# Optimization experiments

Hardware: AMD Instinct MI355X
Metric: run time of the kernel (lower is better)

The kernel has to match this reference:

```python
import jax, jax.numpy as jnp
import numpy as np

N_OPCODES = 31
B, S, D = 64, 16, 1024
MAX_STEPS = 16


def setup_inputs() -> dict:
    key = jax.random.key(0)
    k1, k2, k3, k4 = jax.random.split(key, 4)
    return {
        "opcode_logits": jax.random.normal(k1, (B, S, N_OPCODES), dtype=jnp.float32),
        "operands": jax.random.normal(k2, (B, S, 4), dtype=jnp.float32),
        "signal": jax.random.normal(k3, (B, D), dtype=jnp.float32),
        "op_kernels": jax.random.normal(k4, (N_OPCODES, D, D), dtype=jnp.float32) * 0.01,
    }


def reference(opcode_logits, operands, signal, op_kernels):
    # opcode_logits: (B,S,O), operands: (B,S,4), signal: (B,D), op_kernels: (O,D,D)
    n_steps = min(opcode_logits.shape[1], MAX_STEPS)
    weights = jax.nn.softmax(opcode_logits, axis=-1)  # (B,S,O)

    # time-major inputs for scan: (n_steps, B, O) and (n_steps, B, 1)
    ws = jnp.swapaxes(weights[:, :n_steps], 0, 1)
    gate_logits = jnp.swapaxes(operands[:, :n_steps, 3:4], 0, 1)

    def step(h, inputs):
        w, gl = inputs  # (B,O), (B,1)
        gate = jax.nn.sigmoid(gl)
        # equivalent to h @ (sum_o w_o K_o) but never forms the (B,D,D) kernel
        transformed = jnp.einsum('bo,bd,odk->bk', w, h, op_kernels)
        h_new = gate * transformed + (1.0 - gate) * h
        return h_new, None

    h, _ = jax.lax.scan(step, signal, (ws, gate_logits))
    return h
```

## Files before the change

### kernel.cpp

```cpp
#include <hip/hip_runtime.h>
#include <cstddef>
#include <cstdint>

#define NB 64
#define ND 1024
#define NO 31
#define NSTEPS 16
#define KS 62
#define KT32 992
#define KC32 16

typedef _Float16 half8 __attribute__((ext_vector_type(8)));
typedef float floatx4 __attribute__((ext_vector_type(4)));

__global__ void softmax_k(const float* __restrict__ logits, float* __restrict__ W) {
    int row = blockIdx.x * blockDim.x + threadIdx.x;
    if (row >= NB * NSTEPS) return;
    const float* x = logits + (size_t)row * NO;
    float m = -1e30f;
    for (int o = 0; o < NO; ++o) m = fmaxf(m, x[o]);
    float e[NO]; float s = 0.f;
    for (int o = 0; o < NO; ++o) { e[o] = expf(x[o] - m); s += e[o]; }
    float inv = 1.0f / s;
    float* wo = W + (size_t)row * NO;
    for (int o = 0; o < NO; ++o) wo[o] = e[o] * inv;
}

__global__ __launch_bounds__(256) void kconv_k(const float* __restrict__ K,
                                               _Float16* __restrict__ Ktf) {
    __shared__ float tile[32 * 256];
    int kt  = blockIdx.x >> 2;
    int nb4 = blockIdx.x & 3;
    int tid = threadIdx.x;
    int lane = tid & 63, w = tid >> 6;

    {
        const float* src = K + ((size_t)kt * 32) * ND + nb4 * 256;
        #pragma unroll
        for (int i = 0; i < 8; ++i) {
            int r = i * 4 + w;
            int x = lane * 4;
            int xs = x ^ (((r >> 3) & 1) << 4);
            float4 v = *(const float4*)(src + (size_t)r * ND + x);
            *(float4*)&tile[r * 256 + xs] = v;
        }
    }
    __syncthreads();

    int kl0 = (lane >> 4) * 8;
    int swz = ((lane >> 4) & 1) << 4;
    #pragma unroll
    for (int i = 0; i < 4; ++i) {
        int ns_local = i * 4 + w;
        int nl = ns_local * 16 + (lane & 15);
        int xsw = nl ^ swz;
        half8 v;
        #pragma unroll
        for (int j = 0; j < 8; ++j) v[j] = (_Float16)tile[(kl0 + j) * 256 + xsw];
        int ns = nb4 * 16 + ns_local;
        size_t unit = ((size_t)ns * KT32 + kt) * 64 + lane;
        *(half8*)(Ktf + unit * 8) = v;
    }
}

__global__ __launch_bounds__(512) void gemm_k(
    const float* __restrict__ h, const _Float16* __restrict__ Ktf,
    const float* __restrict__ W, float* __restrict__ P, int step)
{
    __shared__ _Float16 lds_a[64 * 512];
    int nb = blockIdx.x;
    int ks = blockIdx.y;
    int tid = threadIdx.x;
    int l = tid & 63, w = tid >> 6;
    int o = ks >> 1;
    int d_base = (ks & 1) * 512;

    {
        int b = tid >> 3, u = tid & 7;
        float wv = W[((size_t)b * NSTEPS + step) * NO + o];
        const float* hb = h + (size_t)b * ND + d_base;
        #pragma unroll
        for (int li = 0; li < 8; ++li) {
            int p = li * 8 + u;
            float4 x0 = *(const float4*)(hb + p * 8);
            float4 x1 = *(const float4*)(hb + p * 8 + 4);
            half8 v;
            v[0] = (_Float16)(x0.x * wv); v[1] = (_Float16)(x0.y * wv);
            v[2] = (_Float16)(x0.z * wv); v[3] = (_Float16)(x0.w * wv);
            v[4] = (_Float16)(x1.x * wv); v[5] = (_Float16)(x1.y * wv);
            v[6] = (_Float16)(x1.z * wv); v[7] = (_Float16)(x1.w * wv);
            *(half8*)&lds_a[(size_t)(p * 64 + b) * 8] = v;
        }
    }
    __syncthreads();

    int ml = l & 15, q = l >> 4;
    int wn = w & 3, kh = w >> 2;
    int ns0 = nb * 16 + wn * 4;
    const half8* Ap = (const half8*)lds_a;

    half8 breg[4][8];
    #pragma unroll
    for (int t = 0; t < 4; ++t) {
        const half8* bp = (const half8*)Ktf
            + ((size_t)(ns0 + t) * KT32 + (size_t)(ks * KC32 + kh * 8)) * 64 + l;
        #pragma unroll
        for (int s = 0; s < 8; ++s) breg[t][s] = bp[(size_t)s * 64];
    }

    floatx4 acc[4][4] = {};
    #pragma unroll
    for (int s = 0; s < 8; ++s) {
        int abase = ((kh * 8 + s) * 4 + q) * 64 + ml;
        half8 a0 = Ap[abase];
        half8 a1 = Ap[abase + 16];
        half8 a2 = Ap[abase + 32];
        half8 a3 = Ap[abase + 48];
        #pragma unroll
        for (int t = 0; t < 4; ++t) {
            acc[t][0] = __builtin_amdgcn_mfma_f32_16x16x32_f16(a0, breg[t][s], acc[t][0], 0, 0, 0);
            acc[t][1] = __builtin_amdgcn_mfma_f32_16x16x32_f16(a1, breg[t][s], acc[t][1], 0, 0, 0);
            acc[t][2] = __builtin_amdgcn_mfma_f32_16x16x32_f16(a2, breg[t][s], acc[t][2], 0, 0, 0);
            acc[t][3] = __builtin_amdgcn_mfma_f32_16x16x32_f16(a3, breg[t][s], acc[t][3], 0, 0, 0);
        }
    }

    __syncthreads();
    floatx4* lred = (floatx4*)lds_a;
    if (kh == 1) {
        #pragma unroll
        for (int t = 0; t < 4; ++t)
            #pragma unroll
            for (int mt = 0; mt < 4; ++mt)
                lred[(t * 4 + mt) * 256 + wn * 64 + l] = acc[t][mt];
    }
    __syncthreads();
    if (kh == 0) {
        float* Pks = P + (size_t)ks * (NB * ND);
        #pragma unroll
        for (int t = 0; t < 4; ++t) {
            int n = (ns0 + t) * 16 + ml;
            #pragma unroll
            for (int mt = 0; mt < 4; ++mt) {
                floatx4 other = lred[(t * 4 + mt) * 256 + wn * 64 + l];
                #pragma unroll
                for (int r = 0; r < 4; ++r) {
                    int b = mt * 16 + q * 4 + r;
                    Pks[(size_t)b * ND + n] = acc[t][mt][r] + other[r];
                }
            }
        }
    }
}

__global__ void update_k(const float* __restrict__ hin, const float* __restrict__ P,
                         const float* __restrict__ operands, float* __restrict__ hout,
                         int step)
{
    __shared__ float red[256];
    int tid = threadIdx.x;
    int w = tid >> 6, lane = tid & 63;
    int j = (w & 1) * 64 + lane;
    int g = blockIdx.x * 128 + j;
    const float* p = P + (size_t)((w >> 1) * 31) * (NB * ND) + g;
    float s = 0.f;
    #pragma unroll
    for (int i = 0; i < 31; ++i) s += p[(size_t)i * (NB * ND)];
    red[(w >> 1) * 128 + j] = s;
    __syncthreads();
    if (tid < 128) {
        float tot = red[tid] + red[tid + 128];
        int g2 = blockIdx.x * 128 + tid;
        int b = g2 >> 10;
        float gl = operands[((size_t)b * NSTEPS + step) * 4 + 3];
        float gt = 1.0f / (1.0f + expf(-gl));
        hout[g2] = gt * tot + (1.0f - gt) * hin[g2];
    }
}

extern "C" void kernel_launch(void* const* d_in, const int* in_sizes, int n_in,
                              void* d_out, int out_size, void* d_ws, size_t ws_size,
                              hipStream_t stream)
{
    const float* logits   = (const float*)d_in[0];
    const float* operands = (const float*)d_in[1];
    const float* signal   = (const float*)d_in[2];
    const float* opk      = (const float*)d_in[3];
    float* out = (float*)d_out;
    char* ws = (char*)d_ws;

    size_t offW = 0;
    size_t offP = 131072;
    size_t offH = offP + (size_t)KS * NB * ND * 4;
    size_t offK = offH + 2ull * NB * ND * 4;

    float*    W  = (float*)(ws + offW);
    float*    P  = (float*)(ws + offP);
    float*    h0 = (float*)(ws + offH);
    float*    h1 = h0 + NB * ND;
    _Float16* Ktf = (_Float16*)(ws + offK);

    softmax_k<<<dim3(4), 256, 0, stream>>>(logits, W);
    kconv_k<<<dim3(3968), 256, 0, stream>>>(opk, Ktf);

    const float* hc = signal;
    float* hn = h0;
    for (int t = 0; t < NSTEPS; ++t) {
        gemm_k<<<dim3(4, KS), 512, 0, stream>>>(hc, Ktf, W, P, t);
        float* dst = (t == NSTEPS - 1) ? out : hn;
        update_k<<<dim3(512), 256, 0, stream>>>(hc, P, operands, dst, t);
        hc = dst;
        hn = (hn == h0) ? h1 : h0;
    }
}
```

Baseline: 524.6 us.

## Drop intra-block K split in gemm, stream B fragments with register double-buffering

The gemm block goes from 512 to 256 threads. Each wave now covers the full 16-step K chunk instead of splitting K across two wave halves. This removes the LDS cross-wave reduction and its two extra barriers. B fragments are no longer all preloaded into registers; they are prefetched one step ahead to overlap global loads with MFMA. The trade-off is fewer waves per block and a longer serial MFMA chain per wave, which can reduce latency hiding across the 248-block grid.

```diff
diff --git a/kernel.cpp b/kernel.cpp
--- a/kernel.cpp
+++ b/kernel.cpp
@@ -63,7 +63,7 @@
     }
 }
 
-__global__ __launch_bounds__(512) void gemm_k(
+__global__ __launch_bounds__(256) void gemm_k(
     const float* __restrict__ h, const _Float16* __restrict__ Ktf,
     const float* __restrict__ W, float* __restrict__ P, int step)
 {
@@ -74,14 +74,22 @@
     int l = tid & 63, w = tid >> 6;
     int o = ks >> 1;
     int d_base = (ks & 1) * 512;
+    int ml = l & 15, q = l >> 4;
+    int ns0 = nb * 16 + w * 4;
+
+    const half8* bp0 = (const half8*)Ktf + ((size_t)(ns0 + 0) * KT32 + (size_t)ks * KC32) * 64 + l;
+    const half8* bp1 = (const half8*)Ktf + ((size_t)(ns0 + 1) * KT32 + (size_t)ks * KC32) * 64 + l;
+    const half8* bp2 = (const half8*)Ktf + ((size_t)(ns0 + 2) * KT32 + (size_t)ks * KC32) * 64 + l;
+    const half8* bp3 = (const half8*)Ktf + ((size_t)(ns0 + 3) * KT32 + (size_t)ks * KC32) * 64 + l;
+    half8 bc0 = bp0[0], bc1 = bp1[0], bc2 = bp2[0], bc3 = bp3[0];
 
     {
-        int b = tid >> 3, u = tid & 7;
-        float wv = W[((size_t)b * NSTEPS + step) * NO + o];
-        const float* hb = h + (size_t)b * ND + d_base;
-        #pragma unroll
-        for (int li = 0; li < 8; ++li) {
-            int p = li * 8 + u;
+        int sb = tid >> 2, su = tid & 3;
+        float wv = W[((size_t)sb * NSTEPS + step) * NO + o];
+        const float* hb = h + (size_t)sb * ND + d_base;
+        #pragma unroll
+        for (int li = 0; li < 16; ++li) {
+            int p = li * 4 + su;
             float4 x0 = *(const float4*)(hb + p * 8);
             float4 x1 = *(const float4*)(hb + p * 8 + 4);
             half8 v;
@@ -89,65 +97,56 @@
             v[2] = (_Float16)(x0.z * wv); v[3] = (_Float16)(x0.w * wv);
             v[4] = (_Float16)(x1.x * wv); v[5] = (_Float16)(x1.y * wv);
             v[6] = (_Float16)(x1.z * wv); v[7] = (_Float16)(x1.w * wv);
-            *(half8*)&lds_a[(size_t)(p * 64 + b) * 8] = v;
+            *(half8*)&lds_a[(size_t)(p * 64 + sb) * 8] = v;
         }
     }
     __syncthreads();
 
-    int ml = l & 15, q = l >> 4;
-    int wn = w & 3, kh = w >> 2;
-    int ns0 = nb * 16 + wn * 4;
     const half8* Ap = (const half8*)lds_a;
-
-    half8 breg[4][8];
-    #pragma unroll
-    for (int t = 0; t < 4; ++t) {
-        const half8* bp = (const half8*)Ktf
-            + ((size_t)(ns0 + t) * KT32 + (size_t)(ks * KC32 + kh * 8)) * 64 + l;
-        #pragma unroll
-        for (int s = 0; s < 8; ++s) breg[t][s] = bp[(size_t)s * 64];
-    }
-
     floatx4 acc[4][4] = {};
     #pragma unroll
-    for (int s = 0; s < 8; ++s) {
-        int abase = ((kh * 8 + s) * 4 + q) * 64 + ml;
+    for (int s = 0; s < KC32; ++s) {
+        half8 bn0, bn1, bn2, bn3;
+        if (s < KC32 - 1) {
+            bn0 = bp0[(size_t)(s + 1) * 64];
+            bn1 = bp1[(size_t)(s + 1) * 64];
+            bn2 = bp2[(size_t)(s + 1) * 64];
+            bn3 = bp3[(size_t)(s + 1) * 64];
+        }
+        int abase = (s * 4 + q) * 64 + ml;
         half8 a0 = Ap[abase];
         half8 a1 = Ap[abase + 16];
         half8 a2 = Ap[abase + 32];
         half8 a3 = Ap[abase + 48];
-        #pragma unroll
-        for (int t = 0; t < 4; ++t) {
-            acc[t][0] = __builtin_amdgcn_mfma_f32_16x16x32_f16(a0, breg[t][s], acc[t][0], 0, 0, 0);
-            acc[t][1] = __builtin_amdgcn_mfma_f32_16x16x32_f16(a1, breg[t][s], acc[t][1], 0, 0, 0);
-            acc[t][2] = __builtin_amdgcn_mfma_f32_16x16x32_f16(a2, breg[t][s], acc[t][2], 0, 0, 0);
-            acc[t][3] = __builtin_amdgcn_mfma_f32_16x16x32_f16(a3, breg[t][s], acc[t][3], 0, 0, 0);
-        }
-    }
-
-    __syncthreads();
-    floatx4* lred = (floatx4*)lds_a;
-    if (kh == 1) {
-        #pragma unroll
-        for (int t = 0; t < 4; ++t)
+        acc[0][0] = __builtin_amdgcn_mfma_f32_16x16x32_f16(a0, bc0, acc[0][0], 0, 0, 0);
+        acc[0][1] = __builtin_amdgcn_mfma_f32_16x16x32_f16(a1, bc0, acc[0][1], 0, 0, 0);
+        acc[0][2] = __builtin_amdgcn_mfma_f32_16x16x32_f16(a2, bc0, acc[0][2], 0, 0, 0);
+        acc[0][3] = __builtin_amdgcn_mfma_f32_16x16x32_f16(a3, bc0, acc[0][3], 0, 0, 0);
+        acc[1][0] = __builtin_amdgcn_mfma_f32_16x16x32_f16(a0, bc1, acc[1][0], 0, 0, 0);
+        acc[1][1] = __builtin_amdgcn_mfma_f32_16x16x32_f16(a1, bc1, acc[1][1], 0, 0, 0);
+        acc[1][2] = __builtin_amdgcn_mfma_f32_16x16x32_f16(a2, bc1, acc[1][2], 0, 0, 0);
+        acc[1][3] = __builtin_amdgcn_mfma_f32_16x16x32_f16(a3, bc1, acc[1][3], 0, 0, 0);
+        acc[2][0] = __builtin_amdgcn_mfma_f32_16x16x32_f16(a0, bc2, acc[2][0], 0, 0, 0);
+        acc[2][1] = __builtin_amdgcn_mfma_f32_16x16x32_f16(a1, bc2, acc[2][1], 0, 0, 0);
+        acc[2][2] = __builtin_amdgcn_mfma_f32_16x16x32_f16(a2, bc2, acc[2][2], 0, 0, 0);
+        acc[2][3] = __builtin_amdgcn_mfma_f32_16x16x32_f16(a3, bc2, acc[2][3], 0, 0, 0);
+        acc[3][0] = __builtin_amdgcn_mfma_f32_16x16x32_f16(a0, bc3, acc[3][0], 0, 0, 0);
+        acc[3][1] = __builtin_amdgcn_mfma_f32_16x16x32_f16(a1, bc3, acc[3][1], 0, 0, 0);
+        acc[3][2] = __builtin_amdgcn_mfma_f32_16x16x32_f16(a2, bc3, acc[3][2], 0, 0, 0);
+        acc[3][3] = __builtin_amdgcn_mfma_f32_16x16x32_f16(a3, bc3, acc[3][3], 0, 0, 0);
+        if (s < KC32 - 1) { bc0 = bn0; bc1 = bn1; bc2 = bn2; bc3 = bn3; }
+    }
+
+    float* Pks = P + (size_t)ks * (NB * ND);
+    #pragma unroll
+    for (int t = 0; t < 4; ++t) {
+        int n = (ns0 + t) * 16 + ml;
+        #pragma unroll
+        for (int mt = 0; mt < 4; ++mt) {
             #pragma unroll
-            for (int mt = 0; mt < 4; ++mt)
-                lred[(t * 4 + mt) * 256 + wn * 64 + l] = acc[t][mt];
-    }
-    __syncthreads();
-    if (kh == 0) {
-        float* Pks = P + (size_t)ks * (NB * ND);
-        #pragma unroll
-        for (int t = 0; t < 4; ++t) {
-            int n = (ns0 + t) * 16 + ml;
-            #pragma unroll
-            for (int mt = 0; mt < 4; ++mt) {
-                floatx4 other = lred[(t * 4 + mt) * 256 + wn * 64 + l];
-                #pragma unroll
-                for (int r = 0; r < 4; ++r) {
-                    int b = mt * 16 + q * 4 + r;
-                    Pks[(size_t)b * ND + n] = acc[t][mt][r] + other[r];
-                }
+            for (int r = 0; r < 4; ++r) {
+                int b = mt * 16 + q * 4 + r;
+                Pks[(size_t)b * ND + n] = acc[t][mt][r];
             }
         }
     }
@@ -206,7 +205,7 @@
     const float* hc = signal;
     float* hn = h0;
     for (int t = 0; t < NSTEPS; ++t) {
-        gemm_k<<<dim3(4, KS), 512, 0, stream>>>(hc, Ktf, W, P, t);
+        gemm_k<<<dim3(4, KS), 256, 0, stream>>>(hc, Ktf, W, P, t);
         float* dst = (t == NSTEPS - 1) ? out : hn;
         update_k<<<dim3(512), 256, 0, stream>>>(hc, P, operands, dst, t);
         hc = dst;
```

Result: no change. 532.6 us (+1.5%).

## Precompute fp16 hidden layout in update kernel, apply opcode weight in GEMM epilogue

Applied to the files above, without the earlier changes.

The update kernel now also writes the new hidden state as fp16 in the MFMA-ready layout, so each GEMM block just copies it into LDS instead of loading fp32, scaling and converting. The opcode weight is applied to the accumulators at store time instead of to the inputs. The GEMM is restructured into 256-thread blocks with a grid twice as wide, each wave owning two N-tiles over the full K range. B fragments are streamed through a two-deep register prefetch, which removes the split-K LDS reduction and its barriers. Risks are lower per-block data reuse, and fp16 rounding of unscaled h in place of weighted h, which changes numerics slightly.

```diff
diff --git a/kernel.cpp b/kernel.cpp
--- a/kernel.cpp
+++ b/kernel.cpp
@@ -8,7 +8,6 @@
 #define NSTEPS 16
 #define KS 62
 #define KT32 992
-#define KC32 16
 
 typedef _Float16 half8 __attribute__((ext_vector_type(8)));
 typedef float floatx4 __attribute__((ext_vector_type(4)));
@@ -26,6 +25,16 @@
     for (int o = 0; o < NO; ++o) wo[o] = e[o] * inv;
 }
 
+__global__ void init16_k(const float* __restrict__ h, _Float16* __restrict__ h16) {
+    int u = blockIdx.x * 256 + threadIdx.x;
+    int d8 = u >> 6, b = u & 63;
+    const float* src = h + (size_t)b * ND + d8 * 8;
+    half8 v;
+    #pragma unroll
+    for (int j = 0; j < 8; ++j) v[j] = (_Float16)src[j];
+    *(half8*)(h16 + (size_t)u * 8) = v;
+}
+
 __global__ __launch_bounds__(256) void kconv_k(const float* __restrict__ K,
                                                _Float16* __restrict__ Ktf) {
     __shared__ float tile[32 * 256];
@@ -63,8 +72,8 @@
     }
 }
 
-__global__ __launch_bounds__(512) void gemm_k(
-    const float* __restrict__ h, const _Float16* __restrict__ Ktf,
+__global__ __launch_bounds__(256) void gemm_k(
+    const _Float16* __restrict__ h16, const _Float16* __restrict__ Ktf,
     const float* __restrict__ W, float* __restrict__ P, int step)
 {
     __shared__ _Float16 lds_a[64 * 512];
@@ -73,81 +82,68 @@
     int tid = threadIdx.x;
     int l = tid & 63, w = tid >> 6;
     int o = ks >> 1;
-    int d_base = (ks & 1) * 512;
+    int ml = l & 15, q = l >> 4;
+    int ns0 = nb * 8 + w * 2;
+
+    const half8* bp0 = (const half8*)Ktf + ((size_t)(ns0 + 0) * KT32 + (size_t)ks * 16) * 64 + l;
+    const half8* bp1 = (const half8*)Ktf + ((size_t)(ns0 + 1) * KT32 + (size_t)ks * 16) * 64 + l;
+    half8 c00 = bp0[0], c10 = bp1[0];
+    half8 c01 = bp0[64], c11 = bp1[64];
 
     {
-        int b = tid >> 3, u = tid & 7;
-        float wv = W[((size_t)b * NSTEPS + step) * NO + o];
-        const float* hb = h + (size_t)b * ND + d_base;
-        #pragma unroll
-        for (int li = 0; li < 8; ++li) {
-            int p = li * 8 + u;
-            float4 x0 = *(const float4*)(hb + p * 8);
-            float4 x1 = *(const float4*)(hb + p * 8 + 4);
-            half8 v;
-            v[0] = (_Float16)(x0.x * wv); v[1] = (_Float16)(x0.y * wv);
-            v[2] = (_Float16)(x0.z * wv); v[3] = (_Float16)(x0.w * wv);
-            v[4] = (_Float16)(x1.x * wv); v[5] = (_Float16)(x1.y * wv);
-            v[6] = (_Float16)(x1.z * wv); v[7] = (_Float16)(x1.w * wv);
-            *(half8*)&lds_a[(size_t)(p * 64 + b) * 8] = v;
+        const half8* hg = (const half8*)h16 + (size_t)(ks & 1) * 4096;
+        #pragma unroll
+        for (int i = 0; i < 16; ++i) {
+            int u = i * 256 + tid;
+            *(half8*)&lds_a[(size_t)u * 8] = hg[u];
         }
     }
     __syncthreads();
 
-    int ml = l & 15, q = l >> 4;
-    int wn = w & 3, kh = w >> 2;
-    int ns0 = nb * 16 + wn * 4;
     const half8* Ap = (const half8*)lds_a;
-
-    half8 breg[4][8];
-    #pragma unroll
-    for (int t = 0; t < 4; ++t) {
-        const half8* bp = (const half8*)Ktf
-            + ((size_t)(ns0 + t) * KT32 + (size_t)(ks * KC32 + kh * 8)) * 64 + l;
-        #pragma unroll
-        for (int s = 0; s < 8; ++s) breg[t][s] = bp[(size_t)s * 64];
-    }
-
-    floatx4 acc[4][4] = {};
-    #pragma unroll
-    for (int s = 0; s < 8; ++s) {
-        int abase = ((kh * 8 + s) * 4 + q) * 64 + ml;
+    floatx4 acc[2][4] = {};
+    #pragma unroll
+    for (int s = 0; s < 16; ++s) {
+        half8 f0, f1;
+        if (s < 14) {
+            f0 = bp0[(size_t)(s + 2) * 64];
+            f1 = bp1[(size_t)(s + 2) * 64];
+        }
+        int abase = (s * 4 + q) * 64 + ml;
         half8 a0 = Ap[abase];
         half8 a1 = Ap[abase + 16];
         half8 a2 = Ap[abase + 32];
         half8 a3 = Ap[abase + 48];
-        #pragma unroll
-        for (int t = 0; t < 4; ++t) {
-            acc[t][0] = __builtin_amdgcn_mfma_f32_16x16x32_f16(a0, breg[t][s], acc[t][0], 0, 0, 0);
-            acc[t][1] = __builtin_amdgcn_mfma_f32_16x16x32_f16(a1, breg[t][s], acc[t][1], 0, 0, 0);
-            acc[t][2] = __builtin_amdgcn_mfma_f32_16x16x32_f16(a2, breg[t][s], acc[t][2], 0, 0, 0);
-            acc[t][3] = __builtin_amdgcn_mfma_f32_16x16x32_f16(a3, breg[t][s], acc[t][3], 0, 0, 0);
-        }
-    }
-
-    __syncthreads();
-    floatx4* lred = (floatx4*)lds_a;
-    if (kh == 1) {
-        #pragma unroll
-        for (int t = 0; t < 4; ++t)
+        acc[0][0] = __builtin_amdgcn_mfma_f32_16x16x32_f16(a0, c00, acc[0][0], 0, 0, 0);
+        acc[0][1] = __builtin_amdgcn_mfma_f32_16x16x32_f16(a1, c00, acc[0][1], 0, 0, 0);
+        acc[0][2] = __builtin_amdgcn_mfma_f32_16x16x32_f16(a2, c00, acc[0][2], 0, 0, 0);
+        acc[0][3] = __builtin_amdgcn_mfma_f32_16x16x32_f16(a3, c00, acc[0][3], 0, 0, 0);
+        acc[1][0] = __builtin_amdgcn_mfma_f32_16x16x32_f16(a0, c10, acc[1][0], 0, 0, 0);
+        acc[1][1] = __builtin_amdgcn_mfma_f32_16x16x32_f16(a1, c10, acc[1][1], 0, 0, 0);
+        acc[1][2] = __builtin_amdgcn_mfma_f32_16x16x32_f16(a2, c10, acc[1][2], 0, 0, 0);
+        acc[1][3] = __builtin_amdgcn_mfma_f32_16x16x32_f16(a3, c10, acc[1][3], 0, 0, 0);
+        if (s < 15) { c00 = c01; c10 = c11; }
+        if (s < 14) { c01 = f0; c11 = f1; }
+    }
+
+    float wtab[16];
+    #pragma unroll
+    for (int mt = 0; mt < 4; ++mt)
+        #pragma unroll
+        for (int r = 0; r < 4; ++r) {
+            int b = mt * 16 + q * 4 + r;
+            wtab[mt * 4 + r] = W[((size_t)b * NSTEPS + step) * NO + o];
+        }
+    float* Pks = P + (size_t)ks * (NB * ND);
+    #pragma unroll
+    for (int tt = 0; tt < 2; ++tt) {
+        int n = (ns0 + tt) * 16 + ml;
+        #pragma unroll
+        for (int mt = 0; mt < 4; ++mt) {
             #pragma unroll
-            for (int mt = 0; mt < 4; ++mt)
-                lred[(t * 4 + mt) * 256 + wn * 64 + l] = acc[t][mt];
-    }
-    __syncthreads();
-    if (kh == 0) {
-        float* Pks = P + (size_t)ks * (NB * ND);
-        #pragma unroll
-        for (int t = 0; t < 4; ++t) {
-            int n = (ns0 + t) * 16 + ml;
-            #pragma unroll
-            for (int mt = 0; mt < 4; ++mt) {
-                floatx4 other = lred[(t * 4 + mt) * 256 + wn * 64 + l];
-                #pragma unroll
-                for (int r = 0; r < 4; ++r) {
-                    int b = mt * 16 + q * 4 + r;
-                    Pks[(size_t)b * ND + n] = acc[t][mt][r] + other[r];
-                }
+            for (int r = 0; r < 4; ++r) {
+                int b = mt * 16 + q * 4 + r;
+                Pks[(size_t)b * ND + n] = acc[tt][mt][r] * wtab[mt * 4 + r];
             }
         }
     }
@@ -155,7 +151,7 @@
 
 __global__ void update_k(const float* __restrict__ hin, const float* __restrict__ P,
                          const float* __restrict__ operands, float* __restrict__ hout,
-                         int step)
+                         _Float16* __restrict__ h16n, int step)
 {
     __shared__ float red[256];
     int tid = threadIdx.x;
@@ -171,10 +167,12 @@
     if (tid < 128) {
         float tot = red[tid] + red[tid + 128];
         int g2 = blockIdx.x * 128 + tid;
-        int b = g2 >> 10;
+        int b = g2 >> 10, n = g2 & 1023;
         float gl = operands[((size_t)b * NSTEPS + step) * 4 + 3];
         float gt = 1.0f / (1.0f + expf(-gl));
-        hout[g2] = gt * tot + (1.0f - gt) * hin[g2];
+        float val = gt * tot + (1.0f - gt) * hin[g2];
+        hout[g2] = val;
+        h16n[((size_t)(n >> 3) * 64 + b) * 8 + (n & 7)] = (_Float16)val;
     }
 }
 
@@ -189,27 +187,34 @@
     float* out = (float*)d_out;
     char* ws = (char*)d_ws;
 
-    size_t offW = 0;
-    size_t offP = 131072;
-    size_t offH = offP + (size_t)KS * NB * ND * 4;
-    size_t offK = offH + 2ull * NB * ND * 4;
-
-    float*    W  = (float*)(ws + offW);
-    float*    P  = (float*)(ws + offP);
-    float*    h0 = (float*)(ws + offH);
-    float*    h1 = h0 + NB * ND;
-    _Float16* Ktf = (_Float16*)(ws + offK);
+    size_t offW   = 0;
+    size_t offP   = 131072;
+    size_t offH   = offP + (size_t)KS * NB * ND * 4;
+    size_t offH16 = offH + 2ull * NB * ND * 4;
+    size_t offK   = offH16 + 2ull * NB * ND * 2;
+
+    float*    W    = (float*)(ws + offW);
+    float*    P    = (float*)(ws + offP);
+    float*    h0   = (float*)(ws + offH);
+    float*    h1   = h0 + NB * ND;
+    _Float16* h16a = (_Float16*)(ws + offH16);
+    _Float16* h16b = h16a + NB * ND;
+    _Float16* Ktf  = (_Float16*)(ws + offK);
 
     softmax_k<<<dim3(4), 256, 0, stream>>>(logits, W);
+    init16_k<<<dim3(32), 256, 0, stream>>>(signal, h16a);
     kconv_k<<<dim3(3968), 256, 0, stream>>>(opk, Ktf);
 
     const float* hc = signal;
     float* hn = h0;
+    _Float16* h16c = h16a;
+    _Float16* h16n = h16b;
     for (int t = 0; t < NSTEPS; ++t) {
-        gemm_k<<<dim3(4, KS), 512, 0, stream>>>(hc, Ktf, W, P, t);
+        gemm_k<<<dim3(8, KS), 256, 0, stream>>>(h16c, Ktf, W, P, t);
         float* dst = (t == NSTEPS - 1) ? out : hn;
-        update_k<<<dim3(512), 256, 0, stream>>>(hc, P, operands, dst, t);
+        update_k<<<dim3(512), 256, 0, stream>>>(hc, P, operands, dst, h16n, t);
         hc = dst;
         hn = (hn == h0) ? h1 : h0;
-    }
-}
+        _Float16* tmp = h16c; h16c = h16n; h16n = tmp;
+    }
+}
```

Measured after the change: 491.7 us. 1.07x faster.
